# Performance work log

Measured on AMD Instinct MI355X. Metric: run time of the kernel, lower is better.

## Reference

```python
import jax, jax.numpy as jnp
import numpy as np

K = 20          # num neighbors (init kwarg k)
BN_EPS = 1e-5   # PyTorch BatchNorm default eps


def setup_inputs() -> dict:
    key = jax.random.key(0)
    k1, k2 = jax.random.split(key, 2)
    x = jax.random.normal(k1, (8, 64, 4096), dtype=jnp.float32)       # (b, d, n)
    w = jax.random.normal(k2, (64, 128), dtype=jnp.float32) * 0.05    # Conv2d 1x1: (out=64, in=2*64)
    gamma = jnp.ones((64,), jnp.float32)    # BatchNorm1d weight
    beta = jnp.zeros((64,), jnp.float32)    # BatchNorm1d bias
    return {"x": x, "w": w, "gamma": gamma, "beta": beta}


def reference(x, w, gamma, beta):
    # x: (b, d, n)
    xt = jnp.swapaxes(x, 1, 2)                       # (b, n, d)
    # kNN via pairwise squared euclidean distance (same ordering as torch.cdist)
    sq = jnp.sum(xt * xt, axis=-1)                   # (b, n)
    d2 = sq[:, :, None] + sq[:, None, :] - 2.0 * jnp.einsum('bnd,bmd->bnm', xt, xt)
    _, idx = jax.lax.top_k(-d2, K)                   # (b, n, K) smallest distances
    # gather neighbor features: (b, n, K, d)
    nb = jax.vmap(lambda pts, i: pts[i])(xt, idx)
    ctr = xt[:, :, None, :]                          # (b, n, 1, d)
    # edge feature = concat([neighbor - x, x]) -> (b, n, K, 2d)
    feat = jnp.concatenate([nb - ctr, jnp.broadcast_to(ctr, nb.shape)], axis=-1)
    # 1x1 conv (no bias) then max over neighbors
    h = jnp.max(jnp.einsum('bnkc,oc->bnko', feat, w), axis=2)   # (b, n, out)
    # BatchNorm1d (training mode: batch statistics over (b, n), biased var)
    mean = jnp.mean(h, axis=(0, 1))
    var = jnp.mean((h - mean) ** 2, axis=(0, 1))
    hn = (h - mean) / jnp.sqrt(var + BN_EPS) * gamma + beta
    out = jax.nn.gelu(hn, approximate=False)         # exact GELU (PyTorch default)
    return jnp.swapaxes(out, 1, 2)                   # (b, out, n)
```

## Files before the change

### kernel.cpp

```cpp
#include <hip/hip_runtime.h>

#define BIGF 3.402823466e38f

typedef __attribute__((ext_vector_type(8))) short bf16x8;
typedef __attribute__((ext_vector_type(4))) float f32x4;

__device__ __forceinline__ void gload_lds16u(const unsigned short* g, unsigned short* lds) {
  __builtin_amdgcn_global_load_lds((const __attribute__((address_space(1))) void*)g,
                                   (__attribute__((address_space(3))) void*)lds, 16, 0, 0);
}

__device__ __forceinline__ unsigned short bf16_rne(float f) {
  unsigned int u = __float_as_uint(f);
  return (unsigned short)((u + 0x7fffu + ((u >> 16) & 1u)) >> 16);
}

__global__ __launch_bounds__(256) void k1_pre(const float* __restrict__ x, const float* __restrict__ w,
                                              float* __restrict__ sq, float* __restrict__ y,
                                              float* __restrict__ delta, unsigned short* __restrict__ xhl) {
  __shared__ __align__(16) float xt[64][68];
  __shared__ __align__(16) float ws[128][64];
  const int t = threadIdx.x;
  const int bid = blockIdx.x;
  const int b = bid >> 6;
  const int n0 = (bid & 63) << 6;
  const float* xb = x + (size_t)b * 64 * 4096;

#pragma unroll
  for (int rep = 0; rep < 16; ++rep) {
    int id = rep * 256 + t;
    int d = id >> 6, n = id & 63;
    xt[n][d] = xb[(size_t)d * 4096 + n0 + n];
  }
#pragma unroll
  for (int rep = 0; rep < 32; ++rep) {
    int id = rep * 256 + t;
    int u = id >> 6, dd = id & 63;
    ws[u][dd] = w[(u & 63) * 128 + ((u >> 6) << 6) + dd];
  }
  __syncthreads();

  {
    const int p = t >> 2;
    const int cg = t & 3;
    uint4* orow = (uint4*)xhl + ((size_t)(b << 12) + n0 + p) * 16;
#pragma unroll
    for (int cc = 0; cc < 4; ++cc) {
      const int c = cg * 4 + cc;
      const int kb = (c & 7) * 8;
      const bool lohalf = (c >= 8);
      unsigned int pk[4];
#pragma unroll
      for (int j2 = 0; j2 < 4; ++j2) {
        unsigned short u0, u1;
#pragma unroll
        for (int e = 0; e < 2; ++e) {
          const float xv = xt[p][kb + j2 * 2 + e];
          unsigned short h = bf16_rne(xv);
          unsigned short r;
          if (!lohalf) r = h;
          else r = bf16_rne(xv - __uint_as_float(((unsigned int)h) << 16));
          if (e == 0) u0 = r; else u1 = r;
        }
        pk[j2] = (unsigned int)u0 | ((unsigned int)u1 << 16);
      }
      uint4 v;
      v.x = pk[0]; v.y = pk[1]; v.z = pk[2]; v.w = pk[3];
      orow[c ^ (p & 7)] = v;
    }
  }

  const int p = t & 63;
  const int oc = t >> 6;
  float accy[16], accz[16];
#pragma unroll
  for (int j = 0; j < 16; ++j) { accy[j] = 0.f; accz[j] = 0.f; }

#pragma unroll 4
  for (int d4 = 0; d4 < 16; ++d4) {
    const float4 xv = *(const float4*)&xt[p][d4 * 4];
#pragma unroll
    for (int j = 0; j < 16; ++j) {
      const int o = oc * 16 + j;
      const float4 wy = *(const float4*)&ws[o][d4 * 4];
      const float4 wz = *(const float4*)&ws[o + 64][d4 * 4];
      accy[j] = fmaf(xv.x, wy.x, fmaf(xv.y, wy.y, fmaf(xv.z, wy.z, fmaf(xv.w, wy.w, accy[j]))));
      accz[j] = fmaf(xv.x, wz.x, fmaf(xv.y, wz.y, fmaf(xv.z, wz.z, fmaf(xv.w, wz.w, accz[j]))));
    }
  }

  if (oc == 0) {
    float s = 0.f;
#pragma unroll
    for (int d4 = 0; d4 < 16; ++d4) {
      const float4 v = *(const float4*)&xt[p][d4 * 4];
      s = fmaf(v.x, v.x, fmaf(v.y, v.y, fmaf(v.z, v.z, fmaf(v.w, v.w, s))));
    }
    sq[b * 4096 + n0 + p] = s;
  }

  const size_t row = ((size_t)b * 4096 + n0 + p) * 64 + oc * 16;
#pragma unroll
  for (int j4 = 0; j4 < 4; ++j4) {
    float4 yv = make_float4(accy[j4 * 4], accy[j4 * 4 + 1], accy[j4 * 4 + 2], accy[j4 * 4 + 3]);
    float4 dv = make_float4(accz[j4 * 4] - accy[j4 * 4], accz[j4 * 4 + 1] - accy[j4 * 4 + 1],
                            accz[j4 * 4 + 2] - accy[j4 * 4 + 2], accz[j4 * 4 + 3] - accy[j4 * 4 + 3]);
    *(float4*)&y[row + j4 * 4] = yv;
    *(float4*)&delta[row + j4 * 4] = dv;
  }
}

__global__ __launch_bounds__(256, 2) void k2_knn(const unsigned short* __restrict__ xhl,
                                                 const float* __restrict__ sq,
                                                 int* __restrict__ idx_out) {
  __shared__ __align__(16) float smem[16448];
  const int t = threadIdx.x;
  const int lane = t & 63;
  const int w = t >> 6;
  float* stW = smem + 4096 + (w << 11);
  float* dumpW = smem + 12288 + (w << 10);
  const uint4* As4 = (const uint4*)smem;
  const uint4* St4 = (const uint4*)stW;
  unsigned* bufD = (unsigned*)smem;
  unsigned* bufI = (unsigned*)(smem + 2048);
  unsigned* thrNa = (unsigned*)(smem + 16384);
  volatile unsigned* thrNv = (volatile unsigned*)(smem + 16384);

  const int bid = blockIdx.x;
  const int b = bid >> 6;
  const int n0 = (bid & 63) << 6;
  const int pn = lane & 15, q = lane >> 4;
  const int myn = lane;

  const unsigned short* xr = xhl + ((size_t)(b << 12)) * 128;
  const float* sqb = sq + (b << 12);

  if (t < 64) thrNa[t] = 0x7F7FFFFFu;

  {
    unsigned short* asu = (unsigned short*)smem;
#pragma unroll
    for (int qq = 0; qq < 4; ++qq) {
      const int kk = (w << 2) + qq;
      gload_lds16u(xr + (size_t)n0 * 128 + kk * 512 + lane * 8, asu + kk * 512);
    }
    unsigned short* stu = (unsigned short*)stW;
    const unsigned short* src = xr + (size_t)(w << 5) * 128;
#pragma unroll
    for (int k = 0; k < 8; ++k) gload_lds16u(src + k * 512 + lane * 8, stu + k * 512);
  }
  f32x4 sqm0 = *(const f32x4*)&sqb[(w << 5) + (q << 2)];
  f32x4 sqm1 = *(const f32x4*)&sqb[(w << 5) + 16 + (q << 2)];
  const float sqn = sqb[n0 + myn];
  __builtin_amdgcn_s_waitcnt(0x0F70);
  __syncthreads();

  bf16x8 bfr[4][4];
#pragma unroll
  for (int nt = 0; nt < 4; ++nt)
#pragma unroll
    for (int j = 0; j < 4; ++j)
      bfr[nt][j] = *reinterpret_cast<const bf16x8*>(&As4[((nt << 4) + pn) * 16 + (((j << 2) + q) ^ (pn & 7))]);
  __syncthreads();

  float kd[20];
  int ki[20];
#pragma unroll
  for (int s = 0; s < 20; ++s) { kd[s] = BIGF; ki[s] = -1; }
  const int swz = myn & 3;
  int cnt = 0;

  auto ins = [&](float vd, int vi) {
#pragma unroll
    for (int s = 0; s < 20; ++s) {
      const float od = kd[s];
      const int oi = ki[s];
      const bool lt = vd < od;
      kd[s] = lt ? vd : od;
      ki[s] = lt ? vi : oi;
      vd = lt ? od : vd;
      vi = lt ? oi : vi;
    }
  };

  auto drain = [&]() {
#pragma unroll 1
    for (int j = 0; j < 8; ++j) {
      if (!__any(j < cnt)) break;
      if (j < cnt) {
        const float dv = __uint_as_float(bufD[j * 256 + t]);
        const int iv = (int)bufI[j * 256 + t];
        if (dv < kd[19]) ins(dv, iv);
      }
    }
    cnt = 0;
    atomicMin(&thrNa[myn], __float_as_uint(kd[19]));
  };

  const f32x4 zero4 = {0.f, 0.f, 0.f, 0.f};
  f32x4 acc[4][2];
#pragma unroll
  for (int nt = 0; nt < 4; ++nt) { acc[nt][0] = zero4; acc[nt][1] = zero4; }
  f32x4 sqmN0 = zero4, sqmN1 = zero4;

  for (int kt = 0; kt < 32; ++kt) {
    const int mbase = (w + (kt << 2)) << 5;
    __builtin_amdgcn_s_waitcnt(0x0F70);

    const float thrSh = __uint_as_float(thrNv[myn]);
    const float thrS = fminf(thrSh, kd[19]);
    const float thr2 = (thrS - sqn) + 0.0625f;

    bf16x8 afr0[4], afr1[4];
#pragma unroll
    for (int j = 0; j < 4; ++j)
      afr0[j] = *reinterpret_cast<const bf16x8*>(&St4[pn * 16 + (((j << 2) + q) ^ (pn & 7))]);
#pragma unroll
    for (int j = 0; j < 4; ++j)
      afr1[j] = *reinterpret_cast<const bf16x8*>(&St4[(16 + pn) * 16 + (((j << 2) + q) ^ (pn & 7))]);
    __builtin_amdgcn_s_waitcnt(0xC07F);

    if (kt < 31) {
      const int mbn = (w + ((kt + 1) << 2)) << 5;
      unsigned short* stu = (unsigned short*)stW;
      const unsigned short* src = xr + (size_t)mbn * 128;
#pragma unroll
      for (int k = 0; k < 8; ++k) gload_lds16u(src + k * 512 + lane * 8, stu + k * 512);
      sqmN0 = *(const f32x4*)&sqb[mbn + (q << 2)];
      sqmN1 = *(const f32x4*)&sqb[mbn + 16 + (q << 2)];
    }

#pragma unroll
    for (int nt = 0; nt < 4; ++nt) {
      f32x4 a = acc[nt][0];
      a = __builtin_amdgcn_mfma_f32_16x16x32_bf16(afr0[0], bfr[nt][0], a, 0, 0, 0);
      a = __builtin_amdgcn_mfma_f32_16x16x32_bf16(afr0[1], bfr[nt][1], a, 0, 0, 0);
      a = __builtin_amdgcn_mfma_f32_16x16x32_bf16(afr0[0], bfr[nt][2], a, 0, 0, 0);
      a = __builtin_amdgcn_mfma_f32_16x16x32_bf16(afr0[1], bfr[nt][3], a, 0, 0, 0);
      a = __builtin_amdgcn_mfma_f32_16x16x32_bf16(afr0[2], bfr[nt][0], a, 0, 0, 0);
      a = __builtin_amdgcn_mfma_f32_16x16x32_bf16(afr0[3], bfr[nt][1], a, 0, 0, 0);
      acc[nt][0] = a;
      f32x4 c = acc[nt][1];
      c = __builtin_amdgcn_mfma_f32_16x16x32_bf16(afr1[0], bfr[nt][0], c, 0, 0, 0);
      c = __builtin_amdgcn_mfma_f32_16x16x32_bf16(afr1[1], bfr[nt][1], c, 0, 0, 0);
      c = __builtin_amdgcn_mfma_f32_16x16x32_bf16(afr1[0], bfr[nt][2], c, 0, 0, 0);
      c = __builtin_amdgcn_mfma_f32_16x16x32_bf16(afr1[1], bfr[nt][3], c, 0, 0, 0);
      c = __builtin_amdgcn_mfma_f32_16x16x32_bf16(afr1[2], bfr[nt][0], c, 0, 0, 0);
      c = __builtin_amdgcn_mfma_f32_16x16x32_bf16(afr1[3], bfr[nt][1], c, 0, 0, 0);
      acc[nt][1] = c;
    }

#pragma unroll
    for (int mt = 0; mt < 2; ++mt) {
      const f32x4 sv = mt ? sqm1 : sqm0;
#pragma unroll
      for (int nt = 0; nt < 4; ++nt) {
        const int n = (nt << 4) + pn;
        const int pc = q ^ (n & 3);
        f32x4 dv = sv - 2.0f * acc[nt][mt];
        *(f32x4*)&dumpW[(n << 4) + (pc << 2)] = dv;
        acc[nt][mt] = zero4;
      }
      const int mb0 = mbase + (mt << 4);
#pragma unroll 1
      for (int cc = 0; cc < 4; ++cc) {
        const float4 v = *(const float4*)&dumpW[(myn << 4) + ((cc ^ swz) << 2)];
        const int mb = mb0 + (cc << 2);
        const float mn = fminf(fminf(v.x, v.y), fminf(v.z, v.w));
        if (mn < thr2) {
          if (v.x < thr2) { bufD[cnt * 256 + t] = __float_as_uint(sqn + v.x); bufI[cnt * 256 + t] = (unsigned)mb; cnt++; }
          if (v.y < thr2) { bufD[cnt * 256 + t] = __float_as_uint(sqn + v.y); bufI[cnt * 256 + t] = (unsigned)(mb + 1); cnt++; }
          if (v.z < thr2) { bufD[cnt * 256 + t] = __float_as_uint(sqn + v.z); bufI[cnt * 256 + t] = (unsigned)(mb + 2); cnt++; }
          if (v.w < thr2) { bufD[cnt * 256 + t] = __float_as_uint(sqn + v.w); bufI[cnt * 256 + t] = (unsigned)(mb + 3); cnt++; }
        }
        if (__any(cnt > 4)) drain();
      }
    }
    sqm0 = sqmN0;
    sqm1 = sqmN1;
  }
  drain();

  __syncthreads();
  float* pf = smem;
  int* pi = (int*)(smem + 5120);
#pragma unroll
  for (int s = 0; s < 20; ++s) {
    pf[(w * 20 + s) * 64 + lane] = kd[s];
    pi[(w * 20 + s) * 64 + lane] = ki[s];
  }
  __syncthreads();
  if (w == 0) {
    auto insTie = [&](float vd, int vi) {
#pragma unroll
      for (int s = 0; s < 20; ++s) {
        const float od = kd[s];
        const int oi = ki[s];
        const bool lt = (vd < od) || (vd == od && vi < oi);
        kd[s] = lt ? vd : od;
        ki[s] = lt ? vi : oi;
        vd = lt ? od : vd;
        vi = lt ? oi : vi;
      }
    };
    for (int ww = 1; ww < 4; ++ww) {
#pragma unroll 1
      for (int s = 0; s < 20; ++s) {
        const float dv = pf[(ww * 20 + s) * 64 + lane];
        const int iv = pi[(ww * 20 + s) * 64 + lane];
        if (dv < kd[19] || (dv == kd[19] && iv < ki[19])) insTie(dv, iv);
      }
    }
    int* orow = idx_out + ((size_t)(b << 12) + n0 + lane) * 20;
#pragma unroll
    for (int s = 0; s < 20; ++s) orow[s] = ki[s];
  }
}

__global__ __launch_bounds__(256) void k3_gather(const float* __restrict__ y,
                                                 const float* __restrict__ delta,
                                                 const int* __restrict__ idx,
                                                 float* __restrict__ h,
                                                 float* __restrict__ sums,
                                                 float* __restrict__ sumsq) {
  const int t = threadIdx.x;
  const int lane = t & 63;
  const int w = t >> 6;
  const int blk = blockIdx.x;
  float s1 = 0.f, s2 = 0.f;
  for (int p = 0; p < 16; ++p) {
    const int ng = blk * 64 + w * 16 + p;
    const int b = ng >> 12;
    const int* row = idx + (size_t)ng * 20;
    float mx = -BIGF;
#pragma unroll
    for (int kk = 0; kk < 20; ++kk) {
      const int nbr = row[kk];
      mx = fmaxf(mx, y[((size_t)(b << 12) + nbr) * 64 + lane]);
    }
    const float hv = mx + delta[(size_t)ng * 64 + lane];
    h[(size_t)ng * 64 + lane] = hv;
    s1 += hv;
    s2 += hv * hv;
  }
  __shared__ float r1[4][64], r2[4][64];
  r1[w][lane] = s1;
  r2[w][lane] = s2;
  __syncthreads();
  if (w == 0) {
    const float a = r1[0][lane] + r1[1][lane] + r1[2][lane] + r1[3][lane];
    const float c = r2[0][lane] + r2[1][lane] + r2[2][lane] + r2[3][lane];
    atomicAdd(&sums[lane], a);
    atomicAdd(&sumsq[lane], c);
  }
}

__global__ __launch_bounds__(256) void k4_bn(const float* __restrict__ h,
                                             const float* __restrict__ sums,
                                             const float* __restrict__ sumsq,
                                             const float* __restrict__ gamma,
                                             const float* __restrict__ beta,
                                             float* __restrict__ out) {
  __shared__ float tile[64][65];
  const int bid = blockIdx.x;
  const int b = bid >> 6;
  const int n0 = (bid & 63) << 6;
  const int t = threadIdx.x;
  const int o = t & 63;
#pragma unroll
  for (int it = 0; it < 16; ++it) {
    const int n = (t >> 6) * 16 + it;
    tile[n][o] = h[(((size_t)b << 12) + n0 + n) * 64 + o];
  }
  __syncthreads();
  const int j = t & 63;
#pragma unroll
  for (int it = 0; it < 16; ++it) {
    const int oo = (t >> 6) * 16 + it;
    const float mean = sums[oo] * (1.0f / 32768.0f);
    const float var = sumsq[oo] * (1.0f / 32768.0f) - mean * mean;
    const float sc = gamma[oo] / sqrtf(var + 1e-5f);
    const float hv = tile[j][oo];
    const float hn = (hv - mean) * sc + beta[oo];
    const float g = 0.5f * hn * (1.0f + erff(hn * 0.70710678118654752f));
    out[((size_t)(b * 64 + oo)) * 4096 + n0 + j] = g;
  }
}

extern "C" void kernel_launch(void* const* d_in, const int* in_sizes, int n_in,
                              void* d_out, int out_size, void* d_ws, size_t ws_size,
                              hipStream_t stream) {
  const float* x = (const float*)d_in[0];
  const float* w = (const float*)d_in[1];
  const float* gamma = (const float*)d_in[2];
  const float* beta = (const float*)d_in[3];
  float* out = (float*)d_out;

  float* sq_ws = (float*)d_ws;
  float* y_ws = sq_ws + 32768;
  float* delta_ws = y_ws + 2097152;
  float* h_ws = delta_ws + 2097152;
  int* idx_ws = (int*)(h_ws + 2097152);
  float* sums = (float*)(idx_ws + 655360);
  float* sumsq = sums + 64;
  unsigned short* xhl = (unsigned short*)h_ws;

  hipMemsetAsync(sums, 0, 2 * 64 * sizeof(float), stream);
  k1_pre<<<512, 256, 0, stream>>>(x, w, sq_ws, y_ws, delta_ws, xhl);
  k2_knn<<<512, 256, 0, stream>>>(xhl, sq_ws, idx_ws);
  k3_gather<<<512, 256, 0, stream>>>(y_ws, delta_ws, idx_ws, h_ws, sums, sumsq);
  k4_bn<<<512, 256, 0, stream>>>(h_ws, sums, sumsq, gamma, beta, out);
}
```

Before: 358.3 us.

## Halve kNN query tile per block, reuse staging LDS as dump, raise occupancy

The kNN kernel now processes 32 query points per block instead of 64 and launches 1024 blocks. Each query row is split across two half-waves that each scan half the candidates. The distance dump reuses the candidate staging buffer, which shrinks shared memory enough for 3 blocks per CU. The software prefetch of the next candidate tile is removed, so loads are now issued at the start of each iteration. The final merge combines eight partial lists per query instead of four. The aim is more parallelism and occupancy, at the cost of losing the load/compute overlap, doing more merge work, and reloading the candidate data twice as often overall.

```diff
diff --git a/kernel.cpp b/kernel.cpp
--- a/kernel.cpp
+++ b/kernel.cpp
@@ -110,54 +110,49 @@
   }
 }
 
-__global__ __launch_bounds__(256, 2) void k2_knn(const unsigned short* __restrict__ xhl,
+__global__ __launch_bounds__(256, 3) void k2_knn(const unsigned short* __restrict__ xhl,
                                                  const float* __restrict__ sq,
                                                  int* __restrict__ idx_out) {
-  __shared__ __align__(16) float smem[16448];
+  __shared__ __align__(16) float smem[12320];
   const int t = threadIdx.x;
   const int lane = t & 63;
   const int w = t >> 6;
-  float* stW = smem + 4096 + (w << 11);
-  float* dumpW = smem + 12288 + (w << 10);
+  float* stW = smem + 2048 + (w << 11);
   const uint4* As4 = (const uint4*)smem;
   const uint4* St4 = (const uint4*)stW;
   unsigned* bufD = (unsigned*)smem;
-  unsigned* bufI = (unsigned*)(smem + 2048);
-  unsigned* thrNa = (unsigned*)(smem + 16384);
-  volatile unsigned* thrNv = (volatile unsigned*)(smem + 16384);
+  unsigned* bufI = (unsigned*)(smem + 10240);
+  unsigned* thrNa = (unsigned*)(smem + 12288);
+  volatile unsigned* thrNv = (volatile unsigned*)(smem + 12288);
 
   const int bid = blockIdx.x;
-  const int b = bid >> 6;
-  const int n0 = (bid & 63) << 6;
+  const int b = bid >> 7;
+  const int n0 = (bid & 127) << 5;
   const int pn = lane & 15, q = lane >> 4;
-  const int myn = lane;
+  const int myn = lane & 31;
+  const int h = lane >> 5;
+  const int swz = myn & 7;
 
   const unsigned short* xr = xhl + ((size_t)(b << 12)) * 128;
   const float* sqb = sq + (b << 12);
 
-  if (t < 64) thrNa[t] = 0x7F7FFFFFu;
+  if (t < 32) thrNa[t] = 0x7F7FFFFFu;
 
   {
     unsigned short* asu = (unsigned short*)smem;
 #pragma unroll
-    for (int qq = 0; qq < 4; ++qq) {
-      const int kk = (w << 2) + qq;
+    for (int qq = 0; qq < 2; ++qq) {
+      const int kk = (w << 1) + qq;
       gload_lds16u(xr + (size_t)n0 * 128 + kk * 512 + lane * 8, asu + kk * 512);
     }
-    unsigned short* stu = (unsigned short*)stW;
-    const unsigned short* src = xr + (size_t)(w << 5) * 128;
-#pragma unroll
-    for (int k = 0; k < 8; ++k) gload_lds16u(src + k * 512 + lane * 8, stu + k * 512);
-  }
-  f32x4 sqm0 = *(const f32x4*)&sqb[(w << 5) + (q << 2)];
-  f32x4 sqm1 = *(const f32x4*)&sqb[(w << 5) + 16 + (q << 2)];
+  }
   const float sqn = sqb[n0 + myn];
   __builtin_amdgcn_s_waitcnt(0x0F70);
   __syncthreads();
 
-  bf16x8 bfr[4][4];
-#pragma unroll
-  for (int nt = 0; nt < 4; ++nt)
+  bf16x8 bfr[2][4];
+#pragma unroll
+  for (int nt = 0; nt < 2; ++nt)
 #pragma unroll
     for (int j = 0; j < 4; ++j)
       bfr[nt][j] = *reinterpret_cast<const bf16x8*>(&As4[((nt << 4) + pn) * 16 + (((j << 2) + q) ^ (pn & 7))]);
@@ -167,7 +162,6 @@
   int ki[20];
 #pragma unroll
   for (int s = 0; s < 20; ++s) { kd[s] = BIGF; ki[s] = -1; }
-  const int swz = myn & 3;
   int cnt = 0;
 
   auto ins = [&](float vd, int vi) {
@@ -198,13 +192,17 @@
   };
 
   const f32x4 zero4 = {0.f, 0.f, 0.f, 0.f};
-  f32x4 acc[4][2];
-#pragma unroll
-  for (int nt = 0; nt < 4; ++nt) { acc[nt][0] = zero4; acc[nt][1] = zero4; }
-  f32x4 sqmN0 = zero4, sqmN1 = zero4;
 
   for (int kt = 0; kt < 32; ++kt) {
     const int mbase = (w + (kt << 2)) << 5;
+    {
+      unsigned short* stu = (unsigned short*)stW;
+      const unsigned short* src = xr + (size_t)mbase * 128;
+#pragma unroll
+      for (int k = 0; k < 8; ++k) gload_lds16u(src + k * 512 + lane * 8, stu + k * 512);
+    }
+    const f32x4 sqm0 = *(const f32x4*)&sqb[mbase + (q << 2)];
+    const f32x4 sqm1 = *(const f32x4*)&sqb[mbase + 16 + (q << 2)];
     __builtin_amdgcn_s_waitcnt(0x0F70);
 
     const float thrSh = __uint_as_float(thrNv[myn]);
@@ -218,21 +216,11 @@
 #pragma unroll
     for (int j = 0; j < 4; ++j)
       afr1[j] = *reinterpret_cast<const bf16x8*>(&St4[(16 + pn) * 16 + (((j << 2) + q) ^ (pn & 7))]);
-    __builtin_amdgcn_s_waitcnt(0xC07F);
-
-    if (kt < 31) {
-      const int mbn = (w + ((kt + 1) << 2)) << 5;
-      unsigned short* stu = (unsigned short*)stW;
-      const unsigned short* src = xr + (size_t)mbn * 128;
-#pragma unroll
-      for (int k = 0; k < 8; ++k) gload_lds16u(src + k * 512 + lane * 8, stu + k * 512);
-      sqmN0 = *(const f32x4*)&sqb[mbn + (q << 2)];
-      sqmN1 = *(const f32x4*)&sqb[mbn + 16 + (q << 2)];
-    }
-
-#pragma unroll
-    for (int nt = 0; nt < 4; ++nt) {
-      f32x4 a = acc[nt][0];
+
+    f32x4 acc[2][2];
+#pragma unroll
+    for (int nt = 0; nt < 2; ++nt) {
+      f32x4 a = zero4;
       a = __builtin_amdgcn_mfma_f32_16x16x32_bf16(afr0[0], bfr[nt][0], a, 0, 0, 0);
       a = __builtin_amdgcn_mfma_f32_16x16x32_bf16(afr0[1], bfr[nt][1], a, 0, 0, 0);
       a = __builtin_amdgcn_mfma_f32_16x16x32_bf16(afr0[0], bfr[nt][2], a, 0, 0, 0);
@@ -240,7 +228,7 @@
       a = __builtin_amdgcn_mfma_f32_16x16x32_bf16(afr0[2], bfr[nt][0], a, 0, 0, 0);
       a = __builtin_amdgcn_mfma_f32_16x16x32_bf16(afr0[3], bfr[nt][1], a, 0, 0, 0);
       acc[nt][0] = a;
-      f32x4 c = acc[nt][1];
+      f32x4 c = zero4;
       c = __builtin_amdgcn_mfma_f32_16x16x32_bf16(afr1[0], bfr[nt][0], c, 0, 0, 0);
       c = __builtin_amdgcn_mfma_f32_16x16x32_bf16(afr1[1], bfr[nt][1], c, 0, 0, 0);
       c = __builtin_amdgcn_mfma_f32_16x16x32_bf16(afr1[0], bfr[nt][2], c, 0, 0, 0);
@@ -251,21 +239,28 @@
     }
 
 #pragma unroll
-    for (int mt = 0; mt < 2; ++mt) {
-      const f32x4 sv = mt ? sqm1 : sqm0;
-#pragma unroll
-      for (int nt = 0; nt < 4; ++nt) {
+    for (int nt = 0; nt < 2; ++nt) {
+#pragma unroll
+      for (int mt = 0; mt < 2; ++mt) {
         const int n = (nt << 4) + pn;
-        const int pc = q ^ (n & 3);
+        const int g = (mt << 2) + q;
+        const int pc = g ^ (n & 7);
+        const f32x4 sv = mt ? sqm1 : sqm0;
         f32x4 dv = sv - 2.0f * acc[nt][mt];
-        *(f32x4*)&dumpW[(n << 4) + (pc << 2)] = dv;
-        acc[nt][mt] = zero4;
-      }
-      const int mb0 = mbase + (mt << 4);
+        *(f32x4*)&stW[(n << 5) + (pc << 2)] = dv;
+      }
+    }
+
+    {
+      const int cb = h << 2;
+      const float4 v0 = *(const float4*)&stW[(myn << 5) + (((cb + 0) ^ swz) << 2)];
+      const float4 v1 = *(const float4*)&stW[(myn << 5) + (((cb + 1) ^ swz) << 2)];
+      const float4 v2 = *(const float4*)&stW[(myn << 5) + (((cb + 2) ^ swz) << 2)];
+      const float4 v3 = *(const float4*)&stW[(myn << 5) + (((cb + 3) ^ swz) << 2)];
 #pragma unroll 1
-      for (int cc = 0; cc < 4; ++cc) {
-        const float4 v = *(const float4*)&dumpW[(myn << 4) + ((cc ^ swz) << 2)];
-        const int mb = mb0 + (cc << 2);
+      for (int cc2 = 0; cc2 < 4; ++cc2) {
+        const float4 v = (cc2 == 0) ? v0 : (cc2 == 1) ? v1 : (cc2 == 2) ? v2 : v3;
+        const int mb = mbase + ((cb + cc2) << 2);
         const float mn = fminf(fminf(v.x, v.y), fminf(v.z, v.w));
         if (mn < thr2) {
           if (v.x < thr2) { bufD[cnt * 256 + t] = __float_as_uint(sqn + v.x); bufI[cnt * 256 + t] = (unsigned)mb; cnt++; }
@@ -276,8 +271,6 @@
         if (__any(cnt > 4)) drain();
       }
     }
-    sqm0 = sqmN0;
-    sqm1 = sqmN1;
   }
   drain();
 
@@ -290,7 +283,7 @@
     pi[(w * 20 + s) * 64 + lane] = ki[s];
   }
   __syncthreads();
-  if (w == 0) {
+  if (w == 0 && lane < 32) {
     auto insTie = [&](float vd, int vi) {
 #pragma unroll
       for (int s = 0; s < 20; ++s) {
@@ -303,15 +296,19 @@
         vi = lt ? oi : vi;
       }
     };
-    for (int ww = 1; ww < 4; ++ww) {
+    for (int ww = 0; ww < 4; ++ww) {
 #pragma unroll 1
-      for (int s = 0; s < 20; ++s) {
-        const float dv = pf[(ww * 20 + s) * 64 + lane];
-        const int iv = pi[(ww * 20 + s) * 64 + lane];
-        if (dv < kd[19] || (dv == kd[19] && iv < ki[19])) insTie(dv, iv);
-      }
-    }
-    int* orow = idx_out + ((size_t)(b << 12) + n0 + lane) * 20;
+      for (int hh = 0; hh < 2; ++hh) {
+        if (ww == 0 && hh == 0) continue;
+#pragma unroll 1
+        for (int s = 0; s < 20; ++s) {
+          const float dv = pf[(ww * 20 + s) * 64 + (hh << 5) + myn];
+          const int iv = pi[(ww * 20 + s) * 64 + (hh << 5) + myn];
+          if (dv < kd[19] || (dv == kd[19] && iv < ki[19])) insTie(dv, iv);
+        }
+      }
+    }
+    int* orow = idx_out + ((size_t)(b << 12) + n0 + myn) * 20;
 #pragma unroll
     for (int s = 0; s < 20; ++s) orow[s] = ki[s];
   }
@@ -407,7 +404,7 @@
 
   hipMemsetAsync(sums, 0, 2 * 64 * sizeof(float), stream);
   k1_pre<<<512, 256, 0, stream>>>(x, w, sq_ws, y_ws, delta_ws, xhl);
-  k2_knn<<<512, 256, 0, stream>>>(xhl, sq_ws, idx_ws);
+  k2_knn<<<1024, 256, 0, stream>>>(xhl, sq_ws, idx_ws);
   k3_gather<<<512, 256, 0, stream>>>(y_ws, delta_ws, idx_ws, h_ws, sums, sumsq);
   k4_bn<<<512, 256, 0, stream>>>(h_ws, sums, sumsq, gamma, beta, out);
 }
```

New measurement: 505.6 us. 41.1% more time.
